# Performance work log

Hardware: AMD Instinct MI355X
Metric: run time of the kernel (lower is better)

The kernel has to match this reference:

```python
import jax, jax.numpy as jnp
import numpy as np

N_NODES = 100000
N_EDGES = 1600000
D_IN = 128
D_OUT = 128


def setup_inputs() -> dict:
    key = jax.random.key(0)
    k1, k2, k3, k4, k5 = jax.random.split(key, 5)
    features = jax.random.normal(k1, (N_NODES, D_IN), dtype=jnp.float32)
    weight = jax.random.normal(k2, (D_IN, D_OUT), dtype=jnp.float32)
    edge_val = jax.random.uniform(k3, (N_EDGES,), dtype=jnp.float32)
    edge_row = jax.random.randint(k4, (N_EDGES,), 0, N_NODES, dtype=jnp.int32)
    edge_col = jax.random.randint(k5, (N_EDGES,), 0, N_NODES, dtype=jnp.int32)
    return {"features": features, "weight": weight, "edge_val": edge_val,
            "edge_row": edge_row, "edge_col": edge_col}


def reference(features, weight, edge_val, edge_row, edge_col):
    # support = features @ W   (dense GEMM; torch.spmm with dense-strided lhs)
    support = features @ weight  # [N, D_OUT]
    # output = pre @ support   (sparse COO adjacency spmm)
    msgs = edge_val[:, None] * support[edge_col]  # [E, D_OUT] gather
    output = jax.ops.segment_sum(msgs, edge_row, num_segments=N_NODES)  # scatter-add
    # act == 'relu'; dropout p=0.0 is identity
    return jax.nn.relu(output)
```

## Files before the change

kernel.cpp:

```cpp
#include <hip/hip_runtime.h>
#include <hip/hip_bf16.h>


#define N_NODES 100000
#define N_EDGES 1600000
#define D 128
#define GEMM_BLOCKS ((N_NODES + 63) / 64)
#define CHUNK_A 8192
#define NBLK_A ((N_EDGES + CHUNK_A - 1) / CHUNK_A)
#define BUCKETS ((N_NODES + 127) / 128)
#define N_SCAN (BUCKETS * NBLK_A)
#define SCAN_BLK ((N_SCAN + 1023) / 1024)
#define BCAP 4608

typedef __attribute__((ext_vector_type(8))) short short8;
typedef __attribute__((ext_vector_type(4))) float floatx4;
typedef int  iv2 __attribute__((ext_vector_type(2)));
typedef int  iv4 __attribute__((ext_vector_type(4)));
typedef float fv4 __attribute__((ext_vector_type(4)));

union U16B { uint4 u4; short8 s8; uint u[4]; ushort us[8]; };

__device__ __forceinline__ ushort f32_to_bf16(float f) {
    uint b = __float_as_uint(f);
    return (ushort)((b + 0x7FFFu + ((b >> 16) & 1u)) >> 16);
}
__device__ __forceinline__ float bf16_to_f32(ushort u) {
    return __uint_as_float((uint)u << 16);
}

__global__ __launch_bounds__(256) void wconv_kernel(const float* __restrict__ W,
                                                    ushort* __restrict__ WB,
                                                    uint* __restrict__ st) {
    const int o = blockIdx.x * 256 + threadIdx.x;
    if (o < D * D) {
        const int K8 = o >> 10, rem = o & 1023, n = rem >> 3, j = rem & 7;
        WB[o] = f32_to_bf16(W[(K8 * 8 + j) * D + n]);
    }
    if (st && blockIdx.x == 0 && threadIdx.x < 256) st[threadIdx.x] = 0u;
}

__global__ __launch_bounds__(256) void gemm_kernel(const float* __restrict__ feat,
                                                   const ushort* __restrict__ WB,
                                                   ushort* __restrict__ support,
                                                   const int* __restrict__ edge_row,
                                                   int* __restrict__ histT) {
    __shared__ int hist[BUCKETS];
    const int bid = blockIdx.x, tid = threadIdx.x;
    const bool doHist = (histT != nullptr) && (bid < NBLK_A);
    if (doHist) {
        for (int i = tid; i < BUCKETS; i += 256) hist[i] = 0;
    }

    const int wave = tid >> 6, lane = tid & 63;
    const int row0 = bid * 64 + wave * 16;
    const int m = lane & 15, g = lane >> 4;

    if (row0 < N_NODES) {
        floatx4 acc[8];
        const floatx4 z = {0.f, 0.f, 0.f, 0.f};
        #pragma unroll
        for (int t = 0; t < 8; t++) acc[t] = z;

        const float* arow = feat + (size_t)(row0 + m) * D;
        const ushort* wb = WB + g * 1024 + m * 8;
        #pragma unroll
        for (int s = 0; s < 4; s++) {
            float4 a0 = *(const float4*)(arow + s * 32 + g * 8);
            float4 a1 = *(const float4*)(arow + s * 32 + g * 8 + 4);
            U16B a;
            a.us[0] = f32_to_bf16(a0.x); a.us[1] = f32_to_bf16(a0.y);
            a.us[2] = f32_to_bf16(a0.z); a.us[3] = f32_to_bf16(a0.w);
            a.us[4] = f32_to_bf16(a1.x); a.us[5] = f32_to_bf16(a1.y);
            a.us[6] = f32_to_bf16(a1.z); a.us[7] = f32_to_bf16(a1.w);
            #pragma unroll
            for (int t = 0; t < 8; t++) {
                U16B b; b.u4 = *(const uint4*)(wb + s * 4096 + t * 128);
                acc[t] = __builtin_amdgcn_mfma_f32_16x16x32_bf16(b.s8, a.s8, acc[t], 0, 0, 0);
            }
        }
        ushort* srow = support + (size_t)(row0 + m) * D + g * 4;
        #pragma unroll
        for (int t = 0; t < 8; t++) {
            union { ushort us[4]; uint2 u2; } o;
            #pragma unroll
            for (int r = 0; r < 4; r++) o.us[r] = f32_to_bf16(acc[t][r]);
            *(uint2*)(srow + t * 16) = o.u2;
        }
    }

    if (doHist) {
        __syncthreads();
        const int base = bid * CHUNK_A;
        #pragma unroll
        for (int k = 0; k < CHUNK_A / 256; k++) {
            const int e = base + k * 256 + tid;
            if (e < N_EDGES) atomicAdd(&hist[edge_row[e] >> 7], 1);
        }
        __syncthreads();
        for (int i = tid; i < BUCKETS; i += 256) histT[i * NBLK_A + bid] = hist[i];
    }
}

__global__ __launch_bounds__(1024) void scan_kernel(const int* __restrict__ histT,
                                                    int* __restrict__ baseST,
                                                    int* __restrict__ bucketOff,
                                                    uint* __restrict__ st) {
    __shared__ int wsum[16];
    __shared__ int s_run, s_base;
    const int tid = threadIdx.x, b = blockIdx.x;
    const int gid = b * 1024 + tid;
    const int lane = tid & 63, wave = tid >> 6;

    const int v = (gid < N_SCAN) ? histT[gid] : 0;
    int x = v;
    #pragma unroll
    for (int d = 1; d < 64; d <<= 1) {
        int y = __shfl_up(x, d, 64);
        if (lane >= d) x += y;
    }
    if (lane == 63) wsum[wave] = x;
    __syncthreads();
    if (tid == 0) {
        int run = 0;
        #pragma unroll
        for (int w = 0; w < 16; w++) { int t = wsum[w]; wsum[w] = run; run += t; }
        s_run = run;
        __hip_atomic_store(&st[b], (1u << 30) | (uint)run,
                           __ATOMIC_RELEASE, __HIP_MEMORY_SCOPE_AGENT);
    }
    __syncthreads();
    if (wave == 0) {
        int P = 0;
        int base = b;
        bool done = (b == 0);
        while (!done) {
            const int j = base - 1 - lane;
            uint w;
            if (j >= 0) {
                do {
                    w = __hip_atomic_load(&st[j], __ATOMIC_ACQUIRE, __HIP_MEMORY_SCOPE_AGENT);
                } while ((w >> 30) == 0u);
            } else w = 2u << 30;
            const unsigned long long m2 = __ballot((w >> 30) == 2u);
            int contrib;
            if (m2) {
                const int fl = (int)__ffsll(m2) - 1;
                contrib = (lane <= fl) ? (int)(w & 0x3FFFFFFFu) : 0;
                done = true;
            } else {
                contrib = (int)(w & 0x3FFFFFFFu);
                base -= 64;
            }
            #pragma unroll
            for (int mm = 1; mm < 64; mm <<= 1) contrib += __shfl_xor(contrib, mm, 64);
            P += contrib;
        }
        if (lane == 0) {
            __hip_atomic_store(&st[b], (2u << 30) | (uint)(P + s_run),
                               __ATOMIC_RELEASE, __HIP_MEMORY_SCOPE_AGENT);
            s_base = P;
        }
    }
    __syncthreads();
    if (gid < N_SCAN) {
        const int excl = s_base + wsum[wave] + (x - v);
        const int bucket = gid / NBLK_A;
        const int blk = gid - bucket * NBLK_A;
        baseST[blk * BUCKETS + bucket] = excl;
        if (blk == 0) bucketOff[bucket] = excl;
    }
    if (gid == 0) bucketOff[BUCKETS] = N_EDGES;
}

__global__ __launch_bounds__(1024) void binscatter_kernel(const int* __restrict__ edge_row,
                                                          const int* __restrict__ edge_col,
                                                          const float* __restrict__ edge_val,
                                                          const int* __restrict__ baseST,
                                                          iv2* __restrict__ sorted) {
    __shared__ int cur[BUCKETS];
    const int tid = threadIdx.x, blk = blockIdx.x;
    for (int i = tid; i < BUCKETS; i += 1024) cur[i] = baseST[blk * BUCKETS + i];
    __syncthreads();
    const int base = blk * CHUNK_A;
    #pragma unroll
    for (int k = 0; k < CHUNK_A / 1024; k++) {
        const int e = base + k * 1024 + tid;
        if (e < N_EDGES) {
            const int r = edge_row[e];
            const int p = atomicAdd(&cur[r >> 7], 1);
            iv2 pk;
            pk.x = ((r & 127) << 17) | edge_col[e];
            pk.y = __float_as_int(edge_val[e]);
            sorted[p] = pk;
        }
    }
}

__global__ __launch_bounds__(1024) void bucket_accum_kernel(const int* __restrict__ bucketOff,
                                                            const iv2* __restrict__ sorted,
                                                            const ushort* __restrict__ support,
                                                            float* __restrict__ out) {
    __shared__ iv2 sldsE[BCAP];
    __shared__ int cnt[128], rowStart[128], cur[128];
    __shared__ int wtot;
    const int tid = threadIdx.x, b = blockIdx.x;
    const int s = bucketOff[b];
    const int nE = bucketOff[b + 1] - s;

    if (tid < 128) cnt[tid] = 0;
    __syncthreads();
    for (int i = tid; i < nE; i += 1024)
        atomicAdd(&cnt[sorted[s + i].x >> 17], 1);
    __syncthreads();
    const int lane = tid & 63;
    const int myc = (tid < 128) ? cnt[tid] : 0;
    int x = myc;
    #pragma unroll
    for (int d = 1; d < 64; d <<= 1) {
        int y = __shfl_up(x, d, 64);
        if (lane >= d) x += y;
    }
    if (tid == 63) wtot = x;
    __syncthreads();
    if (tid < 128) {
        const int excl = x - myc + ((tid >= 64) ? wtot : 0);
        rowStart[tid] = excl;
        cur[tid] = excl;
    }
    __syncthreads();
    for (int i = tid; i < nE; i += 1024) {
        const iv2 e = sorted[s + i];
        const int rl = e.x >> 17;
        const int p = atomicAdd(&cur[rl], 1);
        sldsE[p] = e;
    }
    __syncthreads();

    const int g = tid >> 4, part = tid & 15;
    #pragma unroll
    for (int t = 0; t < 2; t++) {
        const int rl = g * 2 + t;
        const int grow = (b << 7) + rl;
        if (grow >= N_NODES) break;
        const int rs = rowStart[rl], re = rs + cnt[rl];

        float acc0[8], acc1[8];
        #pragma unroll
        for (int i = 0; i < 8; i++) { acc0[i] = 0.f; acc1[i] = 0.f; }

        int k = rs;
        for (; k + 3 < re; k += 4) {
            const iv2 e0 = sldsE[k], e1 = sldsE[k + 1];
            const iv2 e2 = sldsE[k + 2], e3 = sldsE[k + 3];
            U16B s0; s0.u4 = *(const uint4*)(support + (size_t)(e0.x & 0x1FFFF) * D + part * 8);
            U16B s1; s1.u4 = *(const uint4*)(support + (size_t)(e1.x & 0x1FFFF) * D + part * 8);
            U16B s2; s2.u4 = *(const uint4*)(support + (size_t)(e2.x & 0x1FFFF) * D + part * 8);
            U16B s3; s3.u4 = *(const uint4*)(support + (size_t)(e3.x & 0x1FFFF) * D + part * 8);
            const float v0 = __int_as_float(e0.y);
            const float v1 = __int_as_float(e1.y);
            const float v2 = __int_as_float(e2.y);
            const float v3 = __int_as_float(e3.y);
            #pragma unroll
            for (int i = 0; i < 8; i++) {
                acc0[i] += bf16_to_f32(s0.us[i]) * v0;
                acc1[i] += bf16_to_f32(s1.us[i]) * v1;
                acc0[i] += bf16_to_f32(s2.us[i]) * v2;
                acc1[i] += bf16_to_f32(s3.us[i]) * v3;
            }
        }
        for (; k < re; ++k) {
            const iv2 e0 = sldsE[k];
            U16B s0; s0.u4 = *(const uint4*)(support + (size_t)(e0.x & 0x1FFFF) * D + part * 8);
            const float v0 = __int_as_float(e0.y);
            #pragma unroll
            for (int i = 0; i < 8; i++) acc0[i] += bf16_to_f32(s0.us[i]) * v0;
        }

        fv4 lo, hi;
        lo.x = fmaxf(acc0[0] + acc1[0], 0.f); lo.y = fmaxf(acc0[1] + acc1[1], 0.f);
        lo.z = fmaxf(acc0[2] + acc1[2], 0.f); lo.w = fmaxf(acc0[3] + acc1[3], 0.f);
        hi.x = fmaxf(acc0[4] + acc1[4], 0.f); hi.y = fmaxf(acc0[5] + acc1[5], 0.f);
        hi.z = fmaxf(acc0[6] + acc1[6], 0.f); hi.w = fmaxf(acc0[7] + acc1[7], 0.f);
        float* dst = out + (size_t)grow * D + part * 8;
        __builtin_nontemporal_store(lo, (fv4*)dst);
        __builtin_nontemporal_store(hi, (fv4*)(dst + 4));
    }
}

__global__ __launch_bounds__(256) void zero_f4_kernel(float4* __restrict__ acc, int n4) {
    int i = blockIdx.x * 256 + threadIdx.x;
    if (i < n4) acc[i] = make_float4(0.f, 0.f, 0.f, 0.f);
}
__global__ __launch_bounds__(256) void spmm_kernel(const ushort* __restrict__ support,
                                                   const float* __restrict__ edge_val,
                                                   const int* __restrict__ edge_row,
                                                   const int* __restrict__ edge_col,
                                                   float* __restrict__ out) {
    const long gtid = (long)blockIdx.x * 256 + threadIdx.x;
    const int edge = (int)(gtid >> 4);
    const int part = (int)(gtid & 15);
    if (edge >= N_EDGES) return;
    const int col = edge_col[edge];
    const int row = edge_row[edge];
    const float v = edge_val[edge];
    U16B s; s.u4 = *(const uint4*)(support + (size_t)col * D + part * 8);
    float* dst = out + (size_t)row * D + part * 8;
    #pragma unroll
    for (int i = 0; i < 8; i++) unsafeAtomicAdd(dst + i, bf16_to_f32(s.us[i]) * v);
}
__global__ __launch_bounds__(256) void relu_kernel(float4* __restrict__ out, int n4) {
    int i = blockIdx.x * 256 + threadIdx.x;
    if (i >= n4) return;
    float4 a = out[i];
    a.x = fmaxf(a.x, 0.f); a.y = fmaxf(a.y, 0.f);
    a.z = fmaxf(a.z, 0.f); a.w = fmaxf(a.w, 0.f);
    out[i] = a;
}

extern "C" void kernel_launch(void* const* d_in, const int* in_sizes, int n_in,
                              void* d_out, int out_size, void* d_ws, size_t ws_size,
                              hipStream_t stream) {
    (void)in_sizes; (void)n_in; (void)out_size;
    const float* feat     = (const float*)d_in[0];
    const float* W        = (const float*)d_in[1];
    const float* edge_val = (const float*)d_in[2];
    const int*   edge_row = (const int*)d_in[3];
    const int*   edge_col = (const int*)d_in[4];
    float* out = (float*)d_out;

    char* ws = (char*)d_ws;
    size_t o = 0;
    ushort* support  = (ushort*)(ws + o); o += (size_t)N_NODES * D * sizeof(ushort);
    ushort* WB       = (ushort*)(ws + o); o += (size_t)D * D * sizeof(ushort);
    int*    histT    = (int*)(ws + o);    o += ((size_t)N_SCAN * 4 + 15) & ~15ull;
    int*    baseST   = (int*)(ws + o);    o += ((size_t)N_SCAN * 4 + 15) & ~15ull;
    int*    bucketOff= (int*)(ws + o);    o += ((size_t)(BUCKETS + 1) * 4 + 15) & ~15ull;
    uint*   st       = (uint*)(ws + o);   o += 256 * 4;
    iv2*    sorted   = (iv2*)(ws + o);    o += (size_t)N_EDGES * 8;
    const size_t needed = o;

    if (ws_size >= needed) {
        wconv_kernel<<<(D * D + 255) / 256, 256, 0, stream>>>(W, WB, st);
        gemm_kernel<<<GEMM_BLOCKS, 256, 0, stream>>>(feat, WB, support, edge_row, histT);
        scan_kernel<<<SCAN_BLK, 1024, 0, stream>>>(histT, baseST, bucketOff, st);
        binscatter_kernel<<<NBLK_A, 1024, 0, stream>>>(edge_row, edge_col, edge_val,
                                                       baseST, sorted);
        bucket_accum_kernel<<<BUCKETS, 1024, 0, stream>>>(bucketOff, sorted, support, out);
    } else {
        const int n4 = N_NODES * D / 4;
        zero_f4_kernel<<<(n4 + 255) / 256, 256, 0, stream>>>((float4*)out, n4);
        wconv_kernel<<<(D * D + 255) / 256, 256, 0, stream>>>(W, WB, nullptr);
        gemm_kernel<<<GEMM_BLOCKS, 256, 0, stream>>>(feat, WB, support, nullptr, nullptr);
        spmm_kernel<<<(int)(((long)N_EDGES * 16 + 255) / 256), 256, 0, stream>>>(
            support, edge_val, edge_row, edge_col, out);
        relu_kernel<<<(n4 + 255) / 256, 256, 0, stream>>>((float4*)out, n4);
    }
}
```

Before: 239.3 us.

## Split histogram and GEMM into separate blocks; cache bucket edges in registers

The fused GEMM+histogram kernel now launches extra blocks, so the first NBLK_A blocks only build the row histogram and the rest only run the GEMM. Before, the first blocks did both in sequence. The binscatter loop is unrolled by two so that the loads for two edges are issued before their atomics. The bucket accumulation kernel keeps each thread's up to five edges in registers, so the counting pass and the LDS scatter pass read global memory once instead of twice. The register caching assumes each bucket holds at most 5120 edges, which the later LDS capacity of 4608 already bounds, but the extra registers may reduce occupancy.

```diff
diff --git a/kernel.cpp b/kernel.cpp
--- a/kernel.cpp
+++ b/kernel.cpp
@@ -45,51 +45,10 @@
                                                    ushort* __restrict__ support,
                                                    const int* __restrict__ edge_row,
                                                    int* __restrict__ histT) {
-    __shared__ int hist[BUCKETS];
     const int bid = blockIdx.x, tid = threadIdx.x;
-    const bool doHist = (histT != nullptr) && (bid < NBLK_A);
-    if (doHist) {
+    if (histT != nullptr && bid < NBLK_A) {
+        __shared__ int hist[BUCKETS];
         for (int i = tid; i < BUCKETS; i += 256) hist[i] = 0;
-    }
-
-    const int wave = tid >> 6, lane = tid & 63;
-    const int row0 = bid * 64 + wave * 16;
-    const int m = lane & 15, g = lane >> 4;
-
-    if (row0 < N_NODES) {
-        floatx4 acc[8];
-        const floatx4 z = {0.f, 0.f, 0.f, 0.f};
-        #pragma unroll
-        for (int t = 0; t < 8; t++) acc[t] = z;
-
-        const float* arow = feat + (size_t)(row0 + m) * D;
-        const ushort* wb = WB + g * 1024 + m * 8;
-        #pragma unroll
-        for (int s = 0; s < 4; s++) {
-            float4 a0 = *(const float4*)(arow + s * 32 + g * 8);
-            float4 a1 = *(const float4*)(arow + s * 32 + g * 8 + 4);
-            U16B a;
-            a.us[0] = f32_to_bf16(a0.x); a.us[1] = f32_to_bf16(a0.y);
-            a.us[2] = f32_to_bf16(a0.z); a.us[3] = f32_to_bf16(a0.w);
-            a.us[4] = f32_to_bf16(a1.x); a.us[5] = f32_to_bf16(a1.y);
-            a.us[6] = f32_to_bf16(a1.z); a.us[7] = f32_to_bf16(a1.w);
-            #pragma unroll
-            for (int t = 0; t < 8; t++) {
-                U16B b; b.u4 = *(const uint4*)(wb + s * 4096 + t * 128);
-                acc[t] = __builtin_amdgcn_mfma_f32_16x16x32_bf16(b.s8, a.s8, acc[t], 0, 0, 0);
-            }
-        }
-        ushort* srow = support + (size_t)(row0 + m) * D + g * 4;
-        #pragma unroll
-        for (int t = 0; t < 8; t++) {
-            union { ushort us[4]; uint2 u2; } o;
-            #pragma unroll
-            for (int r = 0; r < 4; r++) o.us[r] = f32_to_bf16(acc[t][r]);
-            *(uint2*)(srow + t * 16) = o.u2;
-        }
-    }
-
-    if (doHist) {
         __syncthreads();
         const int base = bid * CHUNK_A;
         #pragma unroll
@@ -99,6 +58,44 @@
         }
         __syncthreads();
         for (int i = tid; i < BUCKETS; i += 256) histT[i * NBLK_A + bid] = hist[i];
+        return;
+    }
+    const int gbid = (histT != nullptr) ? bid - NBLK_A : bid;
+
+    const int wave = tid >> 6, lane = tid & 63;
+    const int row0 = gbid * 64 + wave * 16;
+    const int m = lane & 15, g = lane >> 4;
+    if (row0 >= N_NODES) return;
+
+    floatx4 acc[8];
+    const floatx4 z = {0.f, 0.f, 0.f, 0.f};
+    #pragma unroll
+    for (int t = 0; t < 8; t++) acc[t] = z;
+
+    const float* arow = feat + (size_t)(row0 + m) * D;
+    const ushort* wb = WB + g * 1024 + m * 8;
+    #pragma unroll
+    for (int s = 0; s < 4; s++) {
+        float4 a0 = *(const float4*)(arow + s * 32 + g * 8);
+        float4 a1 = *(const float4*)(arow + s * 32 + g * 8 + 4);
+        U16B a;
+        a.us[0] = f32_to_bf16(a0.x); a.us[1] = f32_to_bf16(a0.y);
+        a.us[2] = f32_to_bf16(a0.z); a.us[3] = f32_to_bf16(a0.w);
+        a.us[4] = f32_to_bf16(a1.x); a.us[5] = f32_to_bf16(a1.y);
+        a.us[6] = f32_to_bf16(a1.z); a.us[7] = f32_to_bf16(a1.w);
+        #pragma unroll
+        for (int t = 0; t < 8; t++) {
+            U16B b; b.u4 = *(const uint4*)(wb + s * 4096 + t * 128);
+            acc[t] = __builtin_amdgcn_mfma_f32_16x16x32_bf16(b.s8, a.s8, acc[t], 0, 0, 0);
+        }
+    }
+    ushort* srow = support + (size_t)(row0 + m) * D + g * 4;
+    #pragma unroll
+    for (int t = 0; t < 8; t++) {
+        union { ushort us[4]; uint2 u2; } o;
+        #pragma unroll
+        for (int r = 0; r < 4; r++) o.us[r] = f32_to_bf16(acc[t][r]);
+        *(uint2*)(srow + t * 16) = o.u2;
     }
 }
 
@@ -184,14 +181,22 @@
     __syncthreads();
     const int base = blk * CHUNK_A;
     #pragma unroll
-    for (int k = 0; k < CHUNK_A / 1024; k++) {
-        const int e = base + k * 1024 + tid;
-        if (e < N_EDGES) {
-            const int r = edge_row[e];
-            const int p = atomicAdd(&cur[r >> 7], 1);
-            iv2 pk;
-            pk.x = ((r & 127) << 17) | edge_col[e];
-            pk.y = __float_as_int(edge_val[e]);
+    for (int k = 0; k < CHUNK_A / 1024; k += 2) {
+        const int e0 = base + k * 1024 + tid;
+        const int e1 = e0 + 1024;
+        const bool v0 = (e0 < N_EDGES), v1 = (e1 < N_EDGES);
+        int r0 = 0, c0 = 0, r1 = 0, c1 = 0;
+        float w0 = 0.f, w1 = 0.f;
+        if (v0) { r0 = edge_row[e0]; c0 = edge_col[e0]; w0 = edge_val[e0]; }
+        if (v1) { r1 = edge_row[e1]; c1 = edge_col[e1]; w1 = edge_val[e1]; }
+        if (v0) {
+            const int p = atomicAdd(&cur[r0 >> 7], 1);
+            iv2 pk; pk.x = ((r0 & 127) << 17) | c0; pk.y = __float_as_int(w0);
+            sorted[p] = pk;
+        }
+        if (v1) {
+            const int p = atomicAdd(&cur[r1 >> 7], 1);
+            iv2 pk; pk.x = ((r1 & 127) << 17) | c1; pk.y = __float_as_int(w1);
             sorted[p] = pk;
         }
     }
@@ -210,8 +215,24 @@
 
     if (tid < 128) cnt[tid] = 0;
     __syncthreads();
-    for (int i = tid; i < nE; i += 1024)
-        atomicAdd(&cnt[sorted[s + i].x >> 17], 1);
+
+    iv2 h0, h1, h2, h3, h4;
+    {
+        int i = tid;
+        if (i < nE) { h0 = sorted[s + i]; i += 1024; }
+        if (i < nE) { h1 = sorted[s + i]; i += 1024; }
+        if (i < nE) { h2 = sorted[s + i]; i += 1024; }
+        if (i < nE) { h3 = sorted[s + i]; i += 1024; }
+        if (i < nE) { h4 = sorted[s + i]; }
+    }
+    {
+        int i = tid;
+        if (i < nE) { atomicAdd(&cnt[h0.x >> 17], 1); i += 1024; }
+        if (i < nE) { atomicAdd(&cnt[h1.x >> 17], 1); i += 1024; }
+        if (i < nE) { atomicAdd(&cnt[h2.x >> 17], 1); i += 1024; }
+        if (i < nE) { atomicAdd(&cnt[h3.x >> 17], 1); i += 1024; }
+        if (i < nE) { atomicAdd(&cnt[h4.x >> 17], 1); }
+    }
     __syncthreads();
     const int lane = tid & 63;
     const int myc = (tid < 128) ? cnt[tid] : 0;
@@ -229,11 +250,13 @@
         cur[tid] = excl;
     }
     __syncthreads();
-    for (int i = tid; i < nE; i += 1024) {
-        const iv2 e = sorted[s + i];
-        const int rl = e.x >> 17;
-        const int p = atomicAdd(&cur[rl], 1);
-        sldsE[p] = e;
+    {
+        int i = tid;
+        if (i < nE) { sldsE[atomicAdd(&cur[h0.x >> 17], 1)] = h0; i += 1024; }
+        if (i < nE) { sldsE[atomicAdd(&cur[h1.x >> 17], 1)] = h1; i += 1024; }
+        if (i < nE) { sldsE[atomicAdd(&cur[h2.x >> 17], 1)] = h2; i += 1024; }
+        if (i < nE) { sldsE[atomicAdd(&cur[h3.x >> 17], 1)] = h3; i += 1024; }
+        if (i < nE) { sldsE[atomicAdd(&cur[h4.x >> 17], 1)] = h4; }
     }
     __syncthreads();
 
@@ -342,7 +365,8 @@
 
     if (ws_size >= needed) {
         wconv_kernel<<<(D * D + 255) / 256, 256, 0, stream>>>(W, WB, st);
-        gemm_kernel<<<GEMM_BLOCKS, 256, 0, stream>>>(feat, WB, support, edge_row, histT);
+        gemm_kernel<<<NBLK_A + GEMM_BLOCKS, 256, 0, stream>>>(feat, WB, support, edge_row,
+                                                              histT);
         scan_kernel<<<SCAN_BLK, 1024, 0, stream>>>(histT, baseST, bucketOff, st);
         binscatter_kernel<<<NBLK_A, 1024, 0, stream>>>(edge_row, edge_col, edge_val,
                                                        baseST, sorted);
```

Result: faster. 229.9 us, median of 2 (-4.0%).
